# Performance work log

Hardware: AMD Instinct MI355X
Metric: run time of the kernel (lower is better)

The kernel has to match this reference:

```python
import jax, jax.numpy as jnp
import numpy as np

B, S, H, NH = 2, 2048, 2048, 16
HD = H // NH
CLIP_QKV = 8.0
SOFTMAX_SCALE = 1.0 / np.sqrt(HD)
NEG_INF = jnp.finfo(jnp.float32).min


def setup_inputs() -> dict:
    key = jax.random.key(0)
    k1, k2, k3, k4 = jax.random.split(key, 4)
    hidden_states = jax.random.normal(k1, (B, S, H), dtype=jnp.float32)
    position_bias = jax.random.normal(k2, (NH, S, S), dtype=jnp.float32) * 0.1
    # causal mask: True = masked out (upper triangle)
    causal = ~jnp.tril(jnp.ones((S, S), dtype=bool))
    attention_mask = jnp.broadcast_to(causal[None, None], (B, 1, S, S))
    Wqkv = jax.random.normal(k3, (3 * H, H), dtype=jnp.float32) * (1.0 / np.sqrt(H))
    Wout = jax.random.normal(k4, (H, H), dtype=jnp.float32) * (1.0 / np.sqrt(H))
    return {"hidden_states": hidden_states, "position_bias": position_bias,
            "attention_mask": attention_mask, "Wqkv": Wqkv, "Wout": Wout}


def reference(hidden_states, position_bias, attention_mask, Wqkv, Wout):
    # QKV projection (no bias) + clamp
    mixed = hidden_states @ Wqkv.T                        # [B,S,3H]
    mixed = jnp.clip(mixed, -CLIP_QKV, CLIP_QKV)
    q, k, v = jnp.split(mixed, 3, axis=2)
    # [B,S,H] -> [B,NH,S,HD]
    def split_heads(x):
        return x.reshape(B, S, NH, HD).transpose(0, 2, 1, 3)
    q, k, v = split_heads(q), split_heads(k), split_heads(v)
    scores = jnp.einsum('bhqd,bhkd->bhqk', q, k) * SOFTMAX_SCALE
    # full position bias is used (slicing indices are always 0 in source)
    scores = scores + position_bias[None]                 # [B,NH,S,S]
    scores = jnp.where(attention_mask, NEG_INF, scores)
    attn = jax.nn.softmax(scores.astype(jnp.float32), axis=-1).astype(v.dtype)
    ctx = jnp.einsum('bhqk,bhkd->bhqd', attn, v)          # [B,NH,S,HD]
    ctx = ctx.transpose(0, 2, 1, 3).reshape(B, S, H)
    attn_output = ctx @ Wout.T
    return attn_output
```

## Files before the change

### kernel.cpp

```cpp
#include <hip/hip_runtime.h>
#include <hip/hip_bf16.h>
#include <stdint.h>

typedef __bf16 bf16x8 __attribute__((ext_vector_type(8)));
typedef float f32x4 __attribute__((ext_vector_type(4)));

#define SOFTMAX_SCALE 0.08838834764831845f
#define LOG2E 1.44269504088896f

__device__ __forceinline__ bf16x8 load8_cvt(const __hip_bfloat16* p) {
  return *(const bf16x8*)p;
}
__device__ __forceinline__ bf16x8 load8_cvt(const float* p) {
  float4 a = *(const float4*)p;
  float4 b = *(const float4*)(p + 4);
  bf16x8 r;
  r[0] = (__bf16)a.x; r[1] = (__bf16)a.y; r[2] = (__bf16)a.z; r[3] = (__bf16)a.w;
  r[4] = (__bf16)b.x; r[5] = (__bf16)b.y; r[6] = (__bf16)b.z; r[7] = (__bf16)b.w;
  return r;
}

__device__ __forceinline__ void gload_lds16(const __hip_bfloat16* g,
                                            __hip_bfloat16* l) {
  __builtin_amdgcn_global_load_lds(
      (__attribute__((address_space(1))) void*)(g),
      (__attribute__((address_space(3))) void*)(l), 16, 0, 0);
}

__global__ __launch_bounds__(256) void cvt_f32_bf16(
    const float* __restrict__ in, __hip_bfloat16* __restrict__ out, int n8)
{
  int i = blockIdx.x * blockDim.x + threadIdx.x;
  int stride = gridDim.x * blockDim.x;
  for (; i < n8; i += stride)
    *(bf16x8*)(out + (int64_t)i * 8) = load8_cvt(in + (int64_t)i * 8);
}

template <typename TA, typename TB>
__device__ __forceinline__ void gemm_bt_loop(
    const TA* __restrict__ A,
    const TB* __restrict__ B,
    int K, int m0, int n0,
    __hip_bfloat16* As, __hip_bfloat16* Bs,
    f32x4 acc[4][4])
{
  const int t = threadIdx.x;
  const int w = t >> 6, lane = t & 63;
  const int wm = (w >> 1) * 64, wn = (w & 1) * 64;
  const int l16 = lane & 15, quad = lane >> 4;
  constexpr bool ASYNC = (sizeof(TA) == 2) && (sizeof(TB) == 2);

  for (int k0 = 0; k0 < K; k0 += 64) {
    if constexpr (ASYNC) {
      #pragma unroll
      for (int i = 0; i < 4; ++i) {
        int cb = (w * 4 + i) * 64;
        int idx = cb + lane;
        int row = idx >> 3;
        int chs = (idx & 7) ^ (row & 7);
        gload_lds16((const __hip_bfloat16*)A + (int64_t)(m0 + row) * K + k0 + chs * 8,
                    As + cb * 8);
        gload_lds16((const __hip_bfloat16*)B + (int64_t)(n0 + row) * K + k0 + chs * 8,
                    Bs + cb * 8);
      }
    } else {
      #pragma unroll
      for (int i = 0; i < 4; ++i) {
        int idx = i * 256 + t;
        int row = idx >> 3, ch = idx & 7;
        int sw = (ch ^ (row & 7)) * 8;
        *(bf16x8*)(As + row * 64 + sw) =
            load8_cvt(A + (int64_t)(m0 + row) * K + k0 + ch * 8);
        *(bf16x8*)(Bs + row * 64 + sw) =
            load8_cvt(B + (int64_t)(n0 + row) * K + k0 + ch * 8);
      }
    }
    __syncthreads();
    #pragma unroll
    for (int ks = 0; ks < 2; ++ks) {
      bf16x8 af[4], bfr[4];
      #pragma unroll
      for (int mt = 0; mt < 4; ++mt) {
        int row = wm + mt * 16 + l16;
        int ch = ks * 4 + quad;
        af[mt] = *(const bf16x8*)(As + row * 64 + ((ch ^ (row & 7)) * 8));
      }
      #pragma unroll
      for (int nt = 0; nt < 4; ++nt) {
        int row = wn + nt * 16 + l16;
        int ch = ks * 4 + quad;
        bfr[nt] = *(const bf16x8*)(Bs + row * 64 + ((ch ^ (row & 7)) * 8));
      }
      #pragma unroll
      for (int mt = 0; mt < 4; ++mt)
        #pragma unroll
        for (int nt = 0; nt < 4; ++nt)
          acc[mt][nt] = __builtin_amdgcn_mfma_f32_16x16x32_bf16(
              af[mt], bfr[nt], acc[mt][nt], 0, 0, 0);
    }
    __syncthreads();
  }
}

template <typename TA, typename TB>
__global__ __launch_bounds__(256) void qkv_gemm(
    const TA* __restrict__ A,
    const TB* __restrict__ W,
    __hip_bfloat16* __restrict__ qb,
    __hip_bfloat16* __restrict__ kb,
    __hip_bfloat16* __restrict__ vb)
{
  __shared__ __align__(16) __hip_bfloat16 As[128 * 64];
  __shared__ __align__(16) __hip_bfloat16 Bs[128 * 64];
  const f32x4 z4 = {0.f, 0.f, 0.f, 0.f};
  f32x4 acc[4][4];
  #pragma unroll
  for (int mt = 0; mt < 4; ++mt)
    #pragma unroll
    for (int nt = 0; nt < 4; ++nt) acc[mt][nt] = z4;

  const int K = 2048;
  const int n0 = blockIdx.x * 128, m0 = blockIdx.y * 128;
  gemm_bt_loop(A, W, K, m0, n0, As, Bs, acc);

  const int t = threadIdx.x;
  const int w = t >> 6, lane = t & 63;
  const int wm = (w >> 1) * 64, wn = (w & 1) * 64;
  const int l16 = lane & 15, quad = lane >> 4;
  __hip_bfloat16* bufs[3] = {qb, kb, vb};
  #pragma unroll
  for (int nt = 0; nt < 4; ++nt) {
    int gn = n0 + wn + nt * 16 + l16;
    int which = gn >> 11;
    int hc = gn & 2047;
    int head = hc >> 7, d = hc & 127;
    __hip_bfloat16* dst = bufs[which];
    #pragma unroll
    for (int mt = 0; mt < 4; ++mt) {
      #pragma unroll
      for (int r = 0; r < 4; ++r) {
        int gm = m0 + wm + mt * 16 + quad * 4 + r;
        int bb = gm >> 11, s = gm & 2047;
        float val = acc[mt][nt][r];
        val = fminf(8.f, fmaxf(-8.f, val));
        dst[(((int64_t)(bb * 16 + head) * 2048 + s) << 7) + d] =
            __float2bfloat16(val);
      }
    }
  }
}

__global__ __launch_bounds__(256) void transpose_v(
    const __hip_bfloat16* __restrict__ V,
    __hip_bfloat16* __restrict__ Vt)
{
  __shared__ __hip_bfloat16 tile[64][68];
  const int bh = blockIdx.z;
  const int s0 = blockIdx.x * 64;
  const int d0 = blockIdx.y * 64;
  const int t = threadIdx.x;
  const int c = t & 63, rq = t >> 6;
  const __hip_bfloat16* Vp = V + (int64_t)bh * 2048 * 128;
  #pragma unroll
  for (int j = 0; j < 16; ++j) {
    int r = rq * 16 + j;
    tile[r][c] = Vp[(int64_t)(s0 + r) * 128 + d0 + c];
  }
  __syncthreads();
  __hip_bfloat16* Vo = Vt + (int64_t)bh * 128 * 2048;
  #pragma unroll
  for (int j = 0; j < 16; ++j) {
    int dd = rq * 16 + j;
    Vo[(int64_t)(d0 + dd) * 2048 + s0 + c] = tile[c][dd];
  }
}

__device__ __forceinline__ void issue_kv(
    int te,
    const __hip_bfloat16* __restrict__ Kbase,
    const __hip_bfloat16* __restrict__ Vbase,
    __hip_bfloat16* Kn, __hip_bfloat16* Vn, int w, int lane)
{
  const __hip_bfloat16* Kp = Kbase + (int64_t)te * 64 * 128;
  const __hip_bfloat16* Vp = Vbase + te * 64;
  #pragma unroll
  for (int i = 0; i < 4; ++i) {
    int cb = (w * 4 + i) * 64;
    int idx = cb + lane;
    { int row = idx >> 4, chs = (idx & 15) ^ (row & 15);
      gload_lds16(Kp + row * 128 + chs * 8, Kn + cb * 8); }
    { int row = idx >> 3, chs = (idx & 7) ^ (row & 7);
      gload_lds16(Vp + (int64_t)row * 2048 + chs * 8, Vn + cb * 8); }
  }
}

__device__ __forceinline__ void load_bias16(
    const float* __restrict__ bp, int te, float (&b)[16])
{
  const int c = te * 64;
  #pragma unroll
  for (int nt = 0; nt < 4; ++nt)
    #pragma unroll
    for (int r = 0; r < 4; ++r)
      b[nt * 4 + r] = bp[(int64_t)r * 2048 + c + nt * 16];
}

__device__ __forceinline__ void attn_step(
    int kt, int ktmax, int q0,
    const __hip_bfloat16* __restrict__ Kbase,
    const __hip_bfloat16* __restrict__ Vbase,
    const float* __restrict__ bp,
    __hip_bfloat16* __restrict__ Ks,
    __hip_bfloat16* __restrict__ Vs,
    __hip_bfloat16* __restrict__ Ps,
    const bf16x8 (&qf)[4],
    float (&bcur)[16], float (&bnxt)[16],
    f32x4 (&O)[8], float (&m_r)[4], float (&l_r)[4],
    int w, int lane, int l16, int quad)
{
  issue_kv(kt, Kbase, Vbase, Ks, Vs, w, lane);
  __syncthreads();

  const f32x4 z4 = {0.f, 0.f, 0.f, 0.f};
  f32x4 S[4];
  #pragma unroll
  for (int nt = 0; nt < 4; ++nt) S[nt] = z4;
  __builtin_amdgcn_s_setprio(1);
  #pragma unroll
  for (int ks = 0; ks < 4; ++ks) {
    int ch = ks * 4 + quad;
    bf16x8 kf[4];
    #pragma unroll
    for (int nt = 0; nt < 4; ++nt) {
      int row = nt * 16 + l16;
      kf[nt] = *(const bf16x8*)(Ks + row * 128 + ((ch ^ (row & 15)) * 8));
    }
    #pragma unroll
    for (int nt = 0; nt < 4; ++nt)
      S[nt] = __builtin_amdgcn_mfma_f32_16x16x32_bf16(
          qf[ks], kf[nt], S[nt], 0, 0, 0);
  }
  __builtin_amdgcn_s_setprio(0);

  load_bias16(bp, (kt + 1 <= ktmax ? kt + 1 : ktmax), bnxt);

  const bool diag = (kt == ktmax);
  #pragma unroll
  for (int r = 0; r < 4; ++r) {
    int trow = w * 16 + quad * 4 + r;
    int gq = q0 + trow;
    float sv0 = S[0][r] * SOFTMAX_SCALE + bcur[r];
    float sv1 = S[1][r] * SOFTMAX_SCALE + bcur[4 + r];
    float sv2 = S[2][r] * SOFTMAX_SCALE + bcur[8 + r];
    float sv3 = S[3][r] * SOFTMAX_SCALE + bcur[12 + r];
    if (diag) {
      int colb = kt * 64 + l16;
      if (colb      > gq) sv0 = -3.0e38f;
      if (colb + 16 > gq) sv1 = -3.0e38f;
      if (colb + 32 > gq) sv2 = -3.0e38f;
      if (colb + 48 > gq) sv3 = -3.0e38f;
    }
    S[0][r] = sv0; S[1][r] = sv1; S[2][r] = sv2; S[3][r] = sv3;
  }

  #pragma unroll
  for (int r = 0; r < 4; ++r) {
    float rm = fmaxf(fmaxf(S[0][r], S[1][r]), fmaxf(S[2][r], S[3][r]));
    rm = fmaxf(rm, __shfl_xor(rm, 1, 64));
    rm = fmaxf(rm, __shfl_xor(rm, 2, 64));
    rm = fmaxf(rm, __shfl_xor(rm, 4, 64));
    rm = fmaxf(rm, __shfl_xor(rm, 8, 64));
    float mo = m_r[r];
    float mn = fmaxf(mo, rm);
    float alpha = exp2f((mo - mn) * LOG2E);
    float rs = 0.f;
    #pragma unroll
    for (int nt = 0; nt < 4; ++nt) {
      float pv = exp2f((S[nt][r] - mn) * LOG2E);
      S[nt][r] = pv;
      rs += pv;
    }
    rs += __shfl_xor(rs, 1, 64);
    rs += __shfl_xor(rs, 2, 64);
    rs += __shfl_xor(rs, 4, 64);
    rs += __shfl_xor(rs, 8, 64);
    m_r[r] = mn;
    l_r[r] = l_r[r] * alpha + rs;
    #pragma unroll
    for (int nt2 = 0; nt2 < 8; ++nt2) O[nt2][r] *= alpha;
  }

  #pragma unroll
  for (int r = 0; r < 4; ++r) {
    int trow = w * 16 + quad * 4 + r;
    #pragma unroll
    for (int nt = 0; nt < 4; ++nt) {
      int col = nt * 16 + l16;
      Ps[trow * 64 + (((col >> 3) ^ (trow & 7)) << 3) + (col & 7)] =
          __float2bfloat16(S[nt][r]);
    }
  }

  __builtin_amdgcn_s_setprio(1);
  #pragma unroll
  for (int ksp = 0; ksp < 2; ++ksp) {
    int ch = ksp * 4 + quad;
    int prow = w * 16 + l16;
    bf16x8 pf = *(const bf16x8*)(Ps + prow * 64 + ((ch ^ (prow & 7)) * 8));
    #pragma unroll
    for (int nt = 0; nt < 8; ++nt) {
      int row = nt * 16 + l16;
      bf16x8 vf = *(const bf16x8*)(Vs + row * 64 + ((ch ^ (row & 7)) * 8));
      O[nt] = __builtin_amdgcn_mfma_f32_16x16x32_bf16(pf, vf, O[nt], 0, 0, 0);
    }
  }
  __builtin_amdgcn_s_setprio(0);

  __syncthreads();
}

__global__ __launch_bounds__(256, 2) void attn_kernel(
    const __hip_bfloat16* __restrict__ Q,
    const __hip_bfloat16* __restrict__ Kg,
    const __hip_bfloat16* __restrict__ Vt,
    const float* __restrict__ bias,
    __hip_bfloat16* __restrict__ ctx)
{
  __shared__ __align__(16) __hip_bfloat16 Ks[64 * 128];
  __shared__ __align__(16) __hip_bfloat16 Vs[128 * 64];
  __shared__ __align__(16) __hip_bfloat16 Ps[64 * 64];

  const int t = threadIdx.x;
  const int w = t >> 6, lane = t & 63;
  const int l16 = lane & 15, quad = lane >> 4;

  const int y = blockIdx.y;
  const int h = y >> 1, b = y & 1;
  const int bh = b * 16 + h;
  const int qt = (31 - (int)blockIdx.x + 8 * ((y >> 3) & 3)) & 31;
  const int q0 = qt * 64;
  const int ktmax = qt;

  const __hip_bfloat16* Kbase = Kg + (int64_t)bh * 2048 * 128;
  const __hip_bfloat16* Vbase = Vt + (int64_t)bh * 128 * 2048;
  const float* bp = bias + (int64_t)h * 2048 * 2048
                    + (int64_t)(q0 + w * 16 + quad * 4) * 2048 + l16;

  bf16x8 qf[4];
  {
    const __hip_bfloat16* Qp = Q + ((int64_t)bh * 2048 + q0 + w * 16) * 128;
    #pragma unroll
    for (int ks = 0; ks < 4; ++ks)
      qf[ks] = *(const bf16x8*)(Qp + l16 * 128 + ks * 32 + quad * 8);
  }

  const f32x4 z4 = {0.f, 0.f, 0.f, 0.f};
  f32x4 O[8];
  #pragma unroll
  for (int nt = 0; nt < 8; ++nt) O[nt] = z4;
  float m_r[4], l_r[4];
  #pragma unroll
  for (int r = 0; r < 4; ++r) { m_r[r] = -3.0e38f; l_r[r] = 0.f; }

  float bA[16], bB[16];
  load_bias16(bp, 0, bA);

  for (int kt = 0; kt <= ktmax; kt += 2) {
    attn_step(kt, ktmax, q0, Kbase, Vbase, bp, Ks, Vs, Ps, qf,
              bA, bB, O, m_r, l_r, w, lane, l16, quad);
    if (kt + 1 <= ktmax)
      attn_step(kt + 1, ktmax, q0, Kbase, Vbase, bp, Ks, Vs, Ps, qf,
                bB, bA, O, m_r, l_r, w, lane, l16, quad);
  }

  #pragma unroll
  for (int r = 0; r < 4; ++r) {
    int trow = w * 16 + quad * 4 + r;
    int gm = b * 2048 + q0 + trow;
    float inv = 1.f / l_r[r];
    __hip_bfloat16* crow = ctx + (int64_t)gm * 2048 + h * 128;
    #pragma unroll
    for (int nt = 0; nt < 8; ++nt)
      crow[nt * 16 + l16] = __float2bfloat16(O[nt][r] * inv);
  }
}

template <typename TB>
__global__ __launch_bounds__(256) void out_gemm(
    const __hip_bfloat16* __restrict__ A,
    const TB* __restrict__ W,
    float* __restrict__ out)
{
  __shared__ __align__(16) __hip_bfloat16 As[128 * 64];
  __shared__ __align__(16) __hip_bfloat16 Bs[128 * 64];
  const f32x4 z4 = {0.f, 0.f, 0.f, 0.f};
  f32x4 acc[4][4];
  #pragma unroll
  for (int mt = 0; mt < 4; ++mt)
    #pragma unroll
    for (int nt = 0; nt < 4; ++nt) acc[mt][nt] = z4;

  const int K = 2048;
  const int n0 = blockIdx.x * 128, m0 = blockIdx.y * 128;
  gemm_bt_loop(A, W, K, m0, n0, As, Bs, acc);

  const int t = threadIdx.x;
  const int w = t >> 6, lane = t & 63;
  const int wm = (w >> 1) * 64, wn = (w & 1) * 64;
  const int l16 = lane & 15, quad = lane >> 4;
  #pragma unroll
  for (int mt = 0; mt < 4; ++mt) {
    #pragma unroll
    for (int r = 0; r < 4; ++r) {
      int gm = m0 + wm + mt * 16 + quad * 4 + r;
      #pragma unroll
      for (int nt = 0; nt < 4; ++nt) {
        int gn = n0 + wn + nt * 16 + l16;
        out[(int64_t)gm * 2048 + gn] = acc[mt][nt][r];
      }
    }
  }
}

extern "C" void kernel_launch(void* const* d_in, const int* in_sizes, int n_in,
                              void* d_out, int out_size, void* d_ws, size_t ws_size,
                              hipStream_t stream) {
  const float* hs   = (const float*)d_in[0];
  const float* bias = (const float*)d_in[1];
  const float* Wqkv = (const float*)d_in[3];
  const float* Wout = (const float*)d_in[4];
  float* out = (float*)d_out;

  __hip_bfloat16* ws = (__hip_bfloat16*)d_ws;
  const size_t SEG = (size_t)32 * 2048 * 128;
  __hip_bfloat16* q   = ws;
  __hip_bfloat16* k   = ws + SEG;
  __hip_bfloat16* v   = ws + 2 * SEG;
  __hip_bfloat16* vt  = ws + 3 * SEG;
  __hip_bfloat16* ctx = ws + 2 * SEG;

  const size_t NW_QKV = (size_t)6144 * 2048;
  const size_t NW_OUT = (size_t)2048 * 2048;
  const size_t need_bytes = (4 * SEG + NW_QKV + SEG) * sizeof(__hip_bfloat16);

  if (ws_size >= need_bytes) {
    __hip_bfloat16* wqkvb = ws + 4 * SEG;
    __hip_bfloat16* hsb   = wqkvb + NW_QKV;
    __hip_bfloat16* woutb = wqkvb;
    cvt_f32_bf16<<<1024, 256, 0, stream>>>(hs, hsb, (int)(SEG / 8));
    cvt_f32_bf16<<<1024, 256, 0, stream>>>(Wqkv, wqkvb, (int)(NW_QKV / 8));
    qkv_gemm<__hip_bfloat16, __hip_bfloat16>
        <<<dim3(48, 32), 256, 0, stream>>>(hsb, wqkvb, q, k, v);
    transpose_v<<<dim3(32, 2, 32), 256, 0, stream>>>(v, vt);
    cvt_f32_bf16<<<1024, 256, 0, stream>>>(Wout, woutb, (int)(NW_OUT / 8));
    attn_kernel<<<dim3(32, 32), 256, 0, stream>>>(q, k, vt, bias, ctx);
    out_gemm<__hip_bfloat16><<<dim3(16, 32), 256, 0, stream>>>(ctx, woutb, out);
  } else {
    qkv_gemm<float, float><<<dim3(48, 32), 256, 0, stream>>>(hs, Wqkv, q, k, v);
    transpose_v<<<dim3(32, 2, 32), 256, 0, stream>>>(v, vt);
    attn_kernel<<<dim3(32, 32), 256, 0, stream>>>(q, k, vt, bias, ctx);
    out_gemm<float><<<dim3(16, 32), 256, 0, stream>>>(ctx, Wout, out);
  }
}
```

Before: 714.1 us.

## Process paired query tiles per 512-thread block sharing K/V tiles

The attention kernel now uses 512-thread blocks, where two groups of four waves each handle an adjacent 64-row query tile and share every K/V tile loaded into LDS. This halves global K/V load traffic per query row. Each block runs two passes, pairing a long causal range with a short one (15-x and x) to balance work across blocks. The causal mask is now applied on every step instead of only the diagonal tile, which adds compare work. The extra waves on the short query tile also compute on one extra K tile that is fully masked.

```diff
diff --git a/kernel.cpp b/kernel.cpp
--- a/kernel.cpp
+++ b/kernel.cpp
@@ -175,22 +175,22 @@
   }
 }
 
-__device__ __forceinline__ void issue_kv(
+__device__ __forceinline__ void issue_kv8(
     int te,
     const __hip_bfloat16* __restrict__ Kbase,
     const __hip_bfloat16* __restrict__ Vbase,
-    __hip_bfloat16* Kn, __hip_bfloat16* Vn, int w, int lane)
+    __hip_bfloat16* Ks, __hip_bfloat16* Vs, int w, int lane)
 {
   const __hip_bfloat16* Kp = Kbase + (int64_t)te * 64 * 128;
   const __hip_bfloat16* Vp = Vbase + te * 64;
   #pragma unroll
-  for (int i = 0; i < 4; ++i) {
-    int cb = (w * 4 + i) * 64;
+  for (int i = 0; i < 2; ++i) {
+    int cb = (w * 2 + i) * 64;
     int idx = cb + lane;
     { int row = idx >> 4, chs = (idx & 15) ^ (row & 15);
-      gload_lds16(Kp + row * 128 + chs * 8, Kn + cb * 8); }
+      gload_lds16(Kp + row * 128 + chs * 8, Ks + cb * 8); }
     { int row = idx >> 3, chs = (idx & 7) ^ (row & 7);
-      gload_lds16(Vp + (int64_t)row * 2048 + chs * 8, Vn + cb * 8); }
+      gload_lds16(Vp + (int64_t)row * 2048 + chs * 8, Vs + cb * 8); }
   }
 }
 
@@ -206,19 +206,19 @@
 }
 
 __device__ __forceinline__ void attn_step(
-    int kt, int ktmax, int q0,
+    int kt, int ktmax, int q0w,
     const __hip_bfloat16* __restrict__ Kbase,
     const __hip_bfloat16* __restrict__ Vbase,
     const float* __restrict__ bp,
     __hip_bfloat16* __restrict__ Ks,
     __hip_bfloat16* __restrict__ Vs,
-    __hip_bfloat16* __restrict__ Ps,
+    __hip_bfloat16* __restrict__ Psh,
     const bf16x8 (&qf)[4],
     float (&bcur)[16], float (&bnxt)[16],
     f32x4 (&O)[8], float (&m_r)[4], float (&l_r)[4],
-    int w, int lane, int l16, int quad)
-{
-  issue_kv(kt, Kbase, Vbase, Ks, Vs, w, lane);
+    int w, int w4, int lane, int l16, int quad)
+{
+  issue_kv8(kt, Kbase, Vbase, Ks, Vs, w, lane);
   __syncthreads();
 
   const f32x4 z4 = {0.f, 0.f, 0.f, 0.f};
@@ -244,22 +244,18 @@
 
   load_bias16(bp, (kt + 1 <= ktmax ? kt + 1 : ktmax), bnxt);
 
-  const bool diag = (kt == ktmax);
   #pragma unroll
   for (int r = 0; r < 4; ++r) {
-    int trow = w * 16 + quad * 4 + r;
-    int gq = q0 + trow;
+    int gq = q0w + quad * 4 + r;
+    int colb = kt * 64 + l16;
     float sv0 = S[0][r] * SOFTMAX_SCALE + bcur[r];
     float sv1 = S[1][r] * SOFTMAX_SCALE + bcur[4 + r];
     float sv2 = S[2][r] * SOFTMAX_SCALE + bcur[8 + r];
     float sv3 = S[3][r] * SOFTMAX_SCALE + bcur[12 + r];
-    if (diag) {
-      int colb = kt * 64 + l16;
-      if (colb      > gq) sv0 = -3.0e38f;
-      if (colb + 16 > gq) sv1 = -3.0e38f;
-      if (colb + 32 > gq) sv2 = -3.0e38f;
-      if (colb + 48 > gq) sv3 = -3.0e38f;
-    }
+    if (colb      > gq) sv0 = -3.0e38f;
+    if (colb + 16 > gq) sv1 = -3.0e38f;
+    if (colb + 32 > gq) sv2 = -3.0e38f;
+    if (colb + 48 > gq) sv3 = -3.0e38f;
     S[0][r] = sv0; S[1][r] = sv1; S[2][r] = sv2; S[3][r] = sv3;
   }
 
@@ -292,11 +288,11 @@
 
   #pragma unroll
   for (int r = 0; r < 4; ++r) {
-    int trow = w * 16 + quad * 4 + r;
+    int trow = w4 * 16 + quad * 4 + r;
     #pragma unroll
     for (int nt = 0; nt < 4; ++nt) {
       int col = nt * 16 + l16;
-      Ps[trow * 64 + (((col >> 3) ^ (trow & 7)) << 3) + (col & 7)] =
+      Psh[trow * 64 + (((col >> 3) ^ (trow & 7)) << 3) + (col & 7)] =
           __float2bfloat16(S[nt][r]);
     }
   }
@@ -305,8 +301,8 @@
   #pragma unroll
   for (int ksp = 0; ksp < 2; ++ksp) {
     int ch = ksp * 4 + quad;
-    int prow = w * 16 + l16;
-    bf16x8 pf = *(const bf16x8*)(Ps + prow * 64 + ((ch ^ (prow & 7)) * 8));
+    int prow = w4 * 16 + l16;
+    bf16x8 pf = *(const bf16x8*)(Psh + prow * 64 + ((ch ^ (prow & 7)) * 8));
     #pragma unroll
     for (int nt = 0; nt < 8; ++nt) {
       int row = nt * 16 + l16;
@@ -319,7 +315,60 @@
   __syncthreads();
 }
 
-__global__ __launch_bounds__(256, 2) void attn_kernel(
+__device__ __forceinline__ void attn_pass(
+    int pair, int b, int h,
+    const __hip_bfloat16* __restrict__ Q,
+    const __hip_bfloat16* __restrict__ Kbase,
+    const __hip_bfloat16* __restrict__ Vbase,
+    const float* __restrict__ Bb,
+    __hip_bfloat16* __restrict__ ctx,
+    __hip_bfloat16* Ks, __hip_bfloat16* Vs, __hip_bfloat16* Psh,
+    int w, int w4, int lane, int l16, int quad)
+{
+  const int bh = b * 16 + h;
+  const int ktmax = 2 * pair + 1;
+  const int q0w = (2 * pair + (w >> 2)) * 64 + w4 * 16;
+
+  const float* bp = Bb + (int64_t)(q0w + quad * 4) * 2048 + l16;
+
+  bf16x8 qf[4];
+  {
+    const __hip_bfloat16* Qp = Q + ((int64_t)bh * 2048 + q0w) * 128;
+    #pragma unroll
+    for (int ks = 0; ks < 4; ++ks)
+      qf[ks] = *(const bf16x8*)(Qp + l16 * 128 + ks * 32 + quad * 8);
+  }
+
+  const f32x4 z4 = {0.f, 0.f, 0.f, 0.f};
+  f32x4 O[8];
+  #pragma unroll
+  for (int nt = 0; nt < 8; ++nt) O[nt] = z4;
+  float m_r[4], l_r[4];
+  #pragma unroll
+  for (int r = 0; r < 4; ++r) { m_r[r] = -3.0e38f; l_r[r] = 0.f; }
+
+  float bA[16], bB[16];
+  load_bias16(bp, 0, bA);
+
+  for (int kt = 0; kt < ktmax; kt += 2) {
+    attn_step(kt, ktmax, q0w, Kbase, Vbase, bp, Ks, Vs, Psh, qf,
+              bA, bB, O, m_r, l_r, w, w4, lane, l16, quad);
+    attn_step(kt + 1, ktmax, q0w, Kbase, Vbase, bp, Ks, Vs, Psh, qf,
+              bB, bA, O, m_r, l_r, w, w4, lane, l16, quad);
+  }
+
+  #pragma unroll
+  for (int r = 0; r < 4; ++r) {
+    int gm = b * 2048 + q0w + quad * 4 + r;
+    float inv = 1.f / l_r[r];
+    __hip_bfloat16* crow = ctx + (int64_t)gm * 2048 + h * 128;
+    #pragma unroll
+    for (int nt = 0; nt < 8; ++nt)
+      crow[nt * 16 + l16] = __float2bfloat16(O[nt][r] * inv);
+  }
+}
+
+__global__ __launch_bounds__(512, 2) void attn_kernel(
     const __hip_bfloat16* __restrict__ Q,
     const __hip_bfloat16* __restrict__ Kg,
     const __hip_bfloat16* __restrict__ Vt,
@@ -328,61 +377,27 @@
 {
   __shared__ __align__(16) __hip_bfloat16 Ks[64 * 128];
   __shared__ __align__(16) __hip_bfloat16 Vs[128 * 64];
-  __shared__ __align__(16) __hip_bfloat16 Ps[64 * 64];
+  __shared__ __align__(16) __hip_bfloat16 Ps[2 * 64 * 64];
 
   const int t = threadIdx.x;
   const int w = t >> 6, lane = t & 63;
+  const int w4 = w & 3;
   const int l16 = lane & 15, quad = lane >> 4;
 
   const int y = blockIdx.y;
   const int h = y >> 1, b = y & 1;
   const int bh = b * 16 + h;
-  const int qt = (31 - (int)blockIdx.x + 8 * ((y >> 3) & 3)) & 31;
-  const int q0 = qt * 64;
-  const int ktmax = qt;
+  const int x = blockIdx.x;
 
   const __hip_bfloat16* Kbase = Kg + (int64_t)bh * 2048 * 128;
   const __hip_bfloat16* Vbase = Vt + (int64_t)bh * 128 * 2048;
-  const float* bp = bias + (int64_t)h * 2048 * 2048
-                    + (int64_t)(q0 + w * 16 + quad * 4) * 2048 + l16;
-
-  bf16x8 qf[4];
-  {
-    const __hip_bfloat16* Qp = Q + ((int64_t)bh * 2048 + q0 + w * 16) * 128;
-    #pragma unroll
-    for (int ks = 0; ks < 4; ++ks)
-      qf[ks] = *(const bf16x8*)(Qp + l16 * 128 + ks * 32 + quad * 8);
-  }
-
-  const f32x4 z4 = {0.f, 0.f, 0.f, 0.f};
-  f32x4 O[8];
-  #pragma unroll
-  for (int nt = 0; nt < 8; ++nt) O[nt] = z4;
-  float m_r[4], l_r[4];
-  #pragma unroll
-  for (int r = 0; r < 4; ++r) { m_r[r] = -3.0e38f; l_r[r] = 0.f; }
-
-  float bA[16], bB[16];
-  load_bias16(bp, 0, bA);
-
-  for (int kt = 0; kt <= ktmax; kt += 2) {
-    attn_step(kt, ktmax, q0, Kbase, Vbase, bp, Ks, Vs, Ps, qf,
-              bA, bB, O, m_r, l_r, w, lane, l16, quad);
-    if (kt + 1 <= ktmax)
-      attn_step(kt + 1, ktmax, q0, Kbase, Vbase, bp, Ks, Vs, Ps, qf,
-                bB, bA, O, m_r, l_r, w, lane, l16, quad);
-  }
-
-  #pragma unroll
-  for (int r = 0; r < 4; ++r) {
-    int trow = w * 16 + quad * 4 + r;
-    int gm = b * 2048 + q0 + trow;
-    float inv = 1.f / l_r[r];
-    __hip_bfloat16* crow = ctx + (int64_t)gm * 2048 + h * 128;
-    #pragma unroll
-    for (int nt = 0; nt < 8; ++nt)
-      crow[nt * 16 + l16] = __float2bfloat16(O[nt][r] * inv);
-  }
+  const float* Bb = bias + (int64_t)h * 2048 * 2048;
+  __hip_bfloat16* Psh = Ps + (w >> 2) * 64 * 64;
+
+  attn_pass(15 - x, b, h, Q, Kbase, Vbase, Bb, ctx, Ks, Vs, Psh,
+            w, w4, lane, l16, quad);
+  attn_pass(x, b, h, Q, Kbase, Vbase, Bb, ctx, Ks, Vs, Psh,
+            w, w4, lane, l16, quad);
 }
 
 template <typename TB>
@@ -453,12 +468,12 @@
         <<<dim3(48, 32), 256, 0, stream>>>(hsb, wqkvb, q, k, v);
     transpose_v<<<dim3(32, 2, 32), 256, 0, stream>>>(v, vt);
     cvt_f32_bf16<<<1024, 256, 0, stream>>>(Wout, woutb, (int)(NW_OUT / 8));
-    attn_kernel<<<dim3(32, 32), 256, 0, stream>>>(q, k, vt, bias, ctx);
+    attn_kernel<<<dim3(8, 32), 512, 0, stream>>>(q, k, vt, bias, ctx);
     out_gemm<__hip_bfloat16><<<dim3(16, 32), 256, 0, stream>>>(ctx, woutb, out);
   } else {
     qkv_gemm<float, float><<<dim3(48, 32), 256, 0, stream>>>(hs, Wqkv, q, k, v);
     transpose_v<<<dim3(32, 2, 32), 256, 0, stream>>>(v, vt);
-    attn_kernel<<<dim3(32, 32), 256, 0, stream>>>(q, k, vt, bias, ctx);
+    attn_kernel<<<dim3(8, 32), 512, 0, stream>>>(q, k, vt, bias, ctx);
     out_gemm<float><<<dim3(16, 32), 256, 0, stream>>>(ctx, Wout, out);
   }
 }
```

After: 658.1 us. -7.8%, faster.
